# Kernel optimization log

Hardware: AMD Instinct MI355X
Metric: run time of the kernel (lower is better)

Reference implementation:

```python
import jax, jax.numpy as jnp
import numpy as np

B, N, DIM = 4, 1024, 512
H, DH = 8, 64
INNER = H * DH
MLP = 2048
EPS = 1e-5


def layernorm(x, g, b):
    m = x.mean(-1, keepdims=True)
    v = ((x - m) ** 2).mean(-1, keepdims=True)
    return (x - m) / jnp.sqrt(v + EPS) * g + b


def setup_inputs() -> dict:
    key = jax.random.key(0)
    ks = jax.random.split(key, 12)
    s = 0.02
    return {
        "q": jax.random.normal(ks[0], (B, N, DIM), jnp.float32),
        "k": jax.random.normal(ks[1], (B, N, DIM), jnp.float32),
        "v": jax.random.normal(ks[2], (B, N, DIM), jnp.float32),
        "Win": jax.random.normal(ks[3], (INNER, DIM), jnp.float32) * s,
        "Wout": jax.random.normal(ks[4], (DIM, INNER), jnp.float32) * s,
        "bout": jnp.zeros((DIM,), jnp.float32),
        "g1": jnp.ones((DIM,), jnp.float32),
        "b1n": jnp.zeros((DIM,), jnp.float32),
        "g2": jnp.ones((DIM,), jnp.float32),
        "b2n": jnp.zeros((DIM,), jnp.float32),
        "Wup": jax.random.normal(ks[5], (MLP, DIM), jnp.float32) * s,
        "bup": jnp.zeros((MLP,), jnp.float32),
        "Wdn": jax.random.normal(ks[6], (DIM, MLP), jnp.float32) * s,
        "bdn": jnp.zeros((DIM,), jnp.float32),
        "wp_W1": jax.random.normal(ks[7], (DH, 2 * DH), jnp.float32) * s,
        "wp_b1": jnp.zeros((DH,), jnp.float32),
        "wp_g": jnp.ones((DH,), jnp.float32),
        "wp_b": jnp.zeros((DH,), jnp.float32),
        "wp_W2": jax.random.normal(ks[8], (3, DH), jnp.float32) * s,
        "wp_b2": jnp.zeros((3,), jnp.float32),
        "num_heads": H,
        "dim_head": DH,
        "mlp_dim": MLP,
    }


def reference(q, k, v, Win, Wout, bout, g1, b1n, g2, b2n, Wup, bup, Wdn, bdn,
              wp_W1, wp_b1, wp_g, wp_b, wp_W2, wp_b2, num_heads, dim_head, mlp_dim):
    b, n, _ = q.shape

    def split_heads(x):  # [b,n,dim] -> [h,b,n,d]
        f = x @ Win.T
        return f.reshape(b, n, num_heads, dim_head).transpose(2, 0, 1, 3)

    fq = split_heads(layernorm(q, g1, b1n))
    fk = split_heads(layernorm(k, g1, b1n))
    fv = split_heads(layernorm(v, g1, b1n))

    # cosine similarity component
    dots = jnp.einsum('hbnd,hbmd->hbnm', fq, fk)
    nq = jnp.linalg.norm(fq, axis=-1)  # [h,b,n]
    nk = jnp.linalg.norm(fk, axis=-1)  # [h,b,m]
    cosine_sim = dots / (nq[..., :, None] * nk[..., None, :])

    # mean-centered covariance component
    qc = fq - fq.mean(-1, keepdims=True)
    kc = fk - fk.mean(-1, keepdims=True)
    cov_component = jnp.einsum('hbnd,hbmd->hbnm', qc, kc) / dim_head

    # variance outer-product component (torch.var -> unbiased, ddof=1)
    qv = jnp.var(fq, axis=-1, ddof=1)  # [h,b,n]
    kv = jnp.var(fk, axis=-1, ddof=1)  # [h,b,m]
    var_component = qv[..., :, None] * kv[..., None, :] / dim_head

    # dynamic per-head mixing weights
    qg = fq.mean(axis=(1, 2))  # [h,d]
    kg = fk.mean(axis=(1, 2))
    feats = jnp.concatenate([qg, kg], axis=-1)  # [h,2d]
    h1 = jax.nn.relu(layernorm(feats @ wp_W1.T + wp_b1, wp_g, wp_b))
    w = jax.nn.softmax(h1 @ wp_W2.T + wp_b2, axis=-1)  # [h,3]
    cw = w[:, 0][:, None, None, None]
    covw = w[:, 1][:, None, None, None]
    vw = w[:, 2][:, None, None, None]

    scores = cw * cosine_sim + covw * cov_component + vw * var_component
    out = jnp.einsum('hbnm,hbmd->hbnd', scores, fv)
    out = out.transpose(1, 2, 0, 3).reshape(b, n, num_heads * dim_head)
    attn = out @ Wout.T + bout

    q2 = q + attn
    x = layernorm(q2, g2, b2n)
    y = jax.nn.gelu(x @ Wup.T + bup, approximate=False) @ Wdn.T + bdn
    return q2 + y
```

## Files before the change

kernel.cpp:

```cpp
#include <hip/hip_runtime.h>
#include <math.h>

#define EPS 1e-5f
#define ROWS 4096

typedef __attribute__((ext_vector_type(8))) short short8;
typedef __attribute__((ext_vector_type(4))) float floatx4;

__device__ inline short f2bf(float f) {
    unsigned u = __builtin_bit_cast(unsigned, f);
    unsigned r = (u + 0x7fffu + ((u >> 16) & 1u)) >> 16;
    return (short)r;
}

__global__ __launch_bounds__(256) void prep(
    const float* __restrict__ q, const float* __restrict__ k,
    const float* __restrict__ v, const float* __restrict__ g,
    const float* __restrict__ bb, short* __restrict__ qkvout,
    const float* __restrict__ w0, const float* __restrict__ w1,
    const float* __restrict__ w2, const float* __restrict__ w3,
    short* __restrict__ o0, short* __restrict__ o1,
    short* __restrict__ o2, short* __restrict__ o3,
    float* __restrict__ zero0) {
    int bx = blockIdx.x;
    int t = threadIdx.x;
    if (bx < 3072) {
        int tensor = bx >> 10;
        int xb = bx & 1023;
        const float* x = tensor == 0 ? q : (tensor == 1 ? k : v);
        int row = xb * 4 + (t >> 6);
        int col = (t & 63) * 8;
        const float* xr = x + (size_t)row * 512 + col;
        float4 v0 = *(const float4*)xr;
        float4 v1 = *(const float4*)(xr + 4);
        float s = v0.x + v0.y + v0.z + v0.w + v1.x + v1.y + v1.z + v1.w;
        float sq = v0.x * v0.x + v0.y * v0.y + v0.z * v0.z + v0.w * v0.w +
                   v1.x * v1.x + v1.y * v1.y + v1.z * v1.z + v1.w * v1.w;
#pragma unroll
        for (int off = 32; off; off >>= 1) {
            s += __shfl_xor(s, off);
            sq += __shfl_xor(sq, off);
        }
        float m = s * (1.f / 512.f);
        float rstd = rsqrtf(sq * (1.f / 512.f) - m * m + EPS);
        float4 g0 = *(const float4*)(g + col);
        float4 g1 = *(const float4*)(g + col + 4);
        float4 b0 = *(const float4*)(bb + col);
        float4 b1 = *(const float4*)(bb + col + 4);
        short8 o;
        o[0] = f2bf((v0.x - m) * rstd * g0.x + b0.x);
        o[1] = f2bf((v0.y - m) * rstd * g0.y + b0.y);
        o[2] = f2bf((v0.z - m) * rstd * g0.z + b0.z);
        o[3] = f2bf((v0.w - m) * rstd * g0.w + b0.w);
        o[4] = f2bf((v1.x - m) * rstd * g1.x + b1.x);
        o[5] = f2bf((v1.y - m) * rstd * g1.y + b1.y);
        o[6] = f2bf((v1.z - m) * rstd * g1.z + b1.z);
        o[7] = f2bf((v1.w - m) * rstd * g1.w + b1.w);
        *(short8*)(qkvout + (size_t)(tensor * 4096 + row) * 512 + col) = o;
        return;
    }
    if (bx < 4352) {
        int wb = bx - 3072;
        const float* src;
        short* dst;
        int base;
        if (wb < 128) { src = w0; dst = o0; base = wb; }
        else if (wb < 256) { src = w1; dst = o1; base = wb - 128; }
        else if (wb < 768) { src = w2; dst = o2; base = wb - 256; }
        else { src = w3; dst = o3; base = wb - 768; }
        int idx = base * 2048 + t * 8;
        float4 v0 = *(const float4*)(src + idx);
        float4 v1 = *(const float4*)(src + idx + 4);
        short8 o;
        o[0] = f2bf(v0.x); o[1] = f2bf(v0.y); o[2] = f2bf(v0.z); o[3] = f2bf(v0.w);
        o[4] = f2bf(v1.x); o[5] = f2bf(v1.y); o[6] = f2bf(v1.z); o[7] = f2bf(v1.w);
        *(short8*)(dst + idx) = o;
        return;
    }
    int zi = (bx - 4352) * 1024 + t * 4;
    if (zi < 267264) *(float4*)(zero0 + zi) = (float4){0.f, 0.f, 0.f, 0.f};
}

template <int TM, int TN, int EPI, bool OUT_BF16>
__global__ __launch_bounds__(256) void mfma_gemm_nt(
    const short* __restrict__ A, const short* __restrict__ B,
    void* __restrict__ C, int M, int N, int K,
    const float* __restrict__ bias, const float* __restrict__ resid,
    float* __restrict__ Sb, float* __restrict__ qgp, float* __restrict__ kgp) {
    constexpr int FI = TM / 32;
    constexpr int FJ = TN / 32;
    __shared__ short As[TM * 32];
    __shared__ short Bs[TN * 32];
    int t = threadIdx.x;
    int m0 = blockIdx.y * TM, n0 = blockIdx.x * TN;
    int w = t >> 6, lane = t & 63;
    int wm = (w & 1) * (TM / 2), wn = (w >> 1) * (TN / 2);
    floatx4 acc[FI][FJ];
#pragma unroll
    for (int i = 0; i < FI; ++i)
#pragma unroll
        for (int j = 0; j < FJ; ++j) acc[i][j] = (floatx4){0.f, 0.f, 0.f, 0.f};

    int arow = t >> 2, acol = (t & 3) * 8;
    const short* Ag = A + (size_t)(m0 + arow) * K + acol;
    const short* Bg = B + (size_t)(n0 + arow) * K + acol;
    int ldsbase = w * 1024;

    for (int k0 = 0; k0 < K; k0 += 32) {
        __syncthreads();
#pragma unroll
        for (int u = 0; u < TM / 64; ++u)
            __builtin_amdgcn_global_load_lds(
                (const __attribute__((address_space(1))) void*)(Ag + (size_t)u * 64 * K + k0),
                (__attribute__((address_space(3))) void*)((char*)As + u * 4096 + ldsbase),
                16, 0, 0);
#pragma unroll
        for (int u = 0; u < TN / 64; ++u)
            __builtin_amdgcn_global_load_lds(
                (const __attribute__((address_space(1))) void*)(Bg + (size_t)u * 64 * K + k0),
                (__attribute__((address_space(3))) void*)((char*)Bs + u * 4096 + ldsbase),
                16, 0, 0);
        __syncthreads();
        int krow = (lane >> 4) * 8;
        short8 af[FI], bf[FJ];
#pragma unroll
        for (int i = 0; i < FI; ++i)
            af[i] = *(const short8*)&As[(wm + i * 16 + (lane & 15)) * 32 + krow];
#pragma unroll
        for (int j = 0; j < FJ; ++j)
            bf[j] = *(const short8*)&Bs[(wn + j * 16 + (lane & 15)) * 32 + krow];
#pragma unroll
        for (int i = 0; i < FI; ++i)
#pragma unroll
            for (int j = 0; j < FJ; ++j)
                acc[i][j] = __builtin_amdgcn_mfma_f32_16x16x32_bf16(
                    af[i], bf[j], acc[i][j], 0, 0, 0);
    }

    int col = lane & 15, rbase = (lane >> 4) * 4;
#pragma unroll
    for (int i = 0; i < FI; ++i) {
#pragma unroll
        for (int j = 0; j < FJ; ++j) {
            int gcol = n0 + wn + j * 16 + col;
#pragma unroll
            for (int r = 0; r < 4; ++r) {
                int grow = m0 + wm + i * 16 + rbase + r;
                float v = acc[i][j][r];
                if (EPI == 2) v += bias[gcol] + resid[(size_t)grow * N + gcol];
                if (EPI == 3) {
                    v += bias[gcol];
                    v = 0.5f * v * (1.f + erff(v * 0.70710678118654752f));
                }
                if (OUT_BF16)
                    ((short*)C)[(size_t)grow * N + gcol] = f2bf(v);
                else
                    ((float*)C)[(size_t)grow * N + gcol] = v;
            }
        }
    }

    if (EPI == 1) {
        if (m0 < 8192) {
            int tensor = m0 >> 12;
            float* Sbase = Sb + (size_t)tensor * 98304;
            float* dst = tensor ? kgp : qgp;
            int head = (n0 + wn) >> 6;
            int rowbase = (m0 & 4095) + wm;
#pragma unroll
            for (int i = 0; i < FI; ++i) {
#pragma unroll
                for (int r = 0; r < 4; ++r) {
                    float s = 0.f, sq = 0.f;
#pragma unroll
                    for (int j = 0; j < FJ; ++j) {
                        float vv = acc[i][j][r];
                        s += vv;
                        sq += vv * vv;
                    }
#pragma unroll
                    for (int off = 1; off < 16; off <<= 1) {
                        s += __shfl_xor(s, off);
                        sq += __shfl_xor(sq, off);
                    }
                    if ((lane & 15) == 0) {
                        int row = rowbase + i * 16 + rbase + r;
                        int idx = head * ROWS + row;
                        float m = s * (1.f / 64.f);
                        Sbase[idx] = m;
                        Sbase[32768 + idx] = rsqrtf(sq);
                        Sbase[65536 + idx] = (sq - 64.f * m * m) * (1.f / 63.f);
                    }
                }
            }
            float cs[FJ];
#pragma unroll
            for (int j = 0; j < FJ; ++j) {
                float s = 0.f;
#pragma unroll
                for (int i = 0; i < FI; ++i)
#pragma unroll
                    for (int r = 0; r < 4; ++r) s += acc[i][j][r];
                s += __shfl_xor(s, 16);
                s += __shfl_xor(s, 32);
                cs[j] = s;
            }
            if (lane < 16) {
#pragma unroll
                for (int j = 0; j < FJ; ++j)
                    atomicAdd(&dst[head * 64 + j * 16 + lane], cs[j] * (1.f / 4096.f));
            }
        }
    }
}

__global__ __launch_bounds__(256) void lnconv(
    const float* __restrict__ x, const float* __restrict__ g,
    const float* __restrict__ bb, short* __restrict__ out) {
    int t = threadIdx.x;
    int row = blockIdx.x * 4 + (t >> 6);
    int col = (t & 63) * 8;
    const float* xr = x + (size_t)row * 512 + col;
    float4 v0 = *(const float4*)xr;
    float4 v1 = *(const float4*)(xr + 4);
    float s = v0.x + v0.y + v0.z + v0.w + v1.x + v1.y + v1.z + v1.w;
    float sq = v0.x * v0.x + v0.y * v0.y + v0.z * v0.z + v0.w * v0.w +
               v1.x * v1.x + v1.y * v1.y + v1.z * v1.z + v1.w * v1.w;
#pragma unroll
    for (int off = 32; off; off >>= 1) {
        s += __shfl_xor(s, off);
        sq += __shfl_xor(sq, off);
    }
    float m = s * (1.f / 512.f);
    float rstd = rsqrtf(sq * (1.f / 512.f) - m * m + EPS);
    float4 g0 = *(const float4*)(g + col);
    float4 g1 = *(const float4*)(g + col + 4);
    float4 b0 = *(const float4*)(bb + col);
    float4 b1 = *(const float4*)(bb + col + 4);
    short8 o;
    o[0] = f2bf((v0.x - m) * rstd * g0.x + b0.x);
    o[1] = f2bf((v0.y - m) * rstd * g0.y + b0.y);
    o[2] = f2bf((v0.z - m) * rstd * g0.z + b0.z);
    o[3] = f2bf((v0.w - m) * rstd * g0.w + b0.w);
    o[4] = f2bf((v1.x - m) * rstd * g1.x + b1.x);
    o[5] = f2bf((v1.y - m) * rstd * g1.y + b1.y);
    o[6] = f2bf((v1.z - m) * rstd * g1.z + b1.z);
    o[7] = f2bf((v1.w - m) * rstd * g1.w + b1.w);
    *(short8*)(out + (size_t)row * 512 + col) = o;
}

__global__ __launch_bounds__(256) void ksideP(
    const float* __restrict__ fk, const float* __restrict__ fv,
    const float* __restrict__ rnk, const float* __restrict__ kvv,
    const float* __restrict__ mk, float* __restrict__ Mbuf,
    const float* __restrict__ qg, const float* __restrict__ kg,
    const float* __restrict__ W1, const float* __restrict__ b1,
    const float* __restrict__ g, const float* __restrict__ bb,
    const float* __restrict__ W2, const float* __restrict__ b2,
    float* __restrict__ wmix) {
    if (blockIdx.x == 32) {
        int j = threadIdx.x;
        if (j >= 64) return;
        int h = blockIdx.y;
        float acc = 0.f;
        const float* w1r = W1 + j * 128;
        for (int i = 0; i < 64; ++i) acc += qg[h * 64 + i] * w1r[i];
        for (int i = 0; i < 64; ++i) acc += kg[h * 64 + i] * w1r[64 + i];
        acc += b1[j];
        float s = acc, sq = acc * acc;
#pragma unroll
        for (int off = 32; off; off >>= 1) {
            s += __shfl_xor(s, off);
            sq += __shfl_xor(sq, off);
        }
        float m = s * (1.f / 64.f);
        float var = sq * (1.f / 64.f) - m * m;
        float xh = (acc - m) * rsqrtf(var + EPS) * g[j] + bb[j];
        float r = fmaxf(xh, 0.f);
        float l[3];
#pragma unroll
        for (int c = 0; c < 3; ++c) {
            float p = r * W2[c * 64 + j];
#pragma unroll
            for (int off = 32; off; off >>= 1) p += __shfl_xor(p, off);
            l[c] = p + b2[c];
        }
        if (j == 0) {
            float mx = fmaxf(l[0], fmaxf(l[1], l[2]));
            float e0 = expf(l[0] - mx), e1 = expf(l[1] - mx), e2 = expf(l[2] - mx);
            float inv = 1.f / (e0 + e1 + e2);
            wmix[h * 3 + 0] = e0 * inv;
            wmix[h * 3 + 1] = e1 * inv;
            wmix[h * 3 + 2] = e2 * inv;
        }
        return;
    }
    int hb = blockIdx.x;
    int chunk = blockIdx.y;
    int h = hb >> 2, b = hb & 3;
    __shared__ float fkt[2048], fvt[2048];
    __shared__ float rs[32], kvs[32], mks[32];
    int t = threadIdx.x;
    int td = t >> 4, te = t & 15;
    float m1[4][4] = {}, m2[4][4] = {};
    float skv = 0.f, smk = 0.f;
    int mstart = chunk * 128;
    for (int m0 = mstart; m0 < mstart + 128; m0 += 32) {
        __syncthreads();
#pragma unroll
        for (int u = 0; u < 2; ++u) {
            int idx = u * 1024 + t * 4;
            int mm = idx >> 6, d = idx & 63;
            size_t grow = (size_t)(b * 1024 + m0 + mm) * 512 + h * 64 + d;
            *(float4*)&fkt[idx] = *(const float4*)&fk[grow];
            *(float4*)&fvt[idx] = *(const float4*)&fv[grow];
        }
        if (t < 32) {
            int sidx = h * ROWS + b * 1024 + m0 + t;
            rs[t] = rnk[sidx];
            kvs[t] = kvv[sidx];
            mks[t] = mk[sidx];
        }
        __syncthreads();
        for (int mi = 0; mi < 32; ++mi) {
            float r = rs[mi];
            float4 kq = *(const float4*)&fkt[mi * 64 + td * 4];
            float4 vq = *(const float4*)&fvt[mi * 64 + te * 4];
            float kr[4] = {kq.x, kq.y, kq.z, kq.w};
            float vr[4] = {vq.x, vq.y, vq.z, vq.w};
#pragma unroll
            for (int i = 0; i < 4; ++i) {
                float kv_ = kr[i], krr = kv_ * r;
#pragma unroll
                for (int j = 0; j < 4; ++j) {
                    m2[i][j] += kv_ * vr[j];
                    m1[i][j] += krr * vr[j];
                }
            }
            if (t < 64) {
                skv += kvs[mi] * fvt[mi * 64 + t];
                smk += mks[mi] * fvt[mi * 64 + t];
            }
        }
    }
    float* base = Mbuf + (size_t)hb * 8320;
#pragma unroll
    for (int i = 0; i < 4; ++i)
#pragma unroll
        for (int j = 0; j < 4; ++j) {
            atomicAdd(&base[(td * 4 + i) * 64 + te * 4 + j], m1[i][j]);
            atomicAdd(&base[4096 + (td * 4 + i) * 64 + te * 4 + j], m2[i][j]);
        }
    if (t < 64) {
        atomicAdd(&base[8192 + t], skv);
        atomicAdd(&base[8256 + t], smk);
    }
}

__global__ __launch_bounds__(256) void qside(
    const float* __restrict__ fq, const float* __restrict__ Mbuf,
    const float* __restrict__ rnq, const float* __restrict__ mq,
    const float* __restrict__ qv, const float* __restrict__ wmix,
    short* __restrict__ attn_out) {
    int ntile = blockIdx.x, hb = blockIdx.y;
    int h = hb >> 2, b = hb & 3;
    __shared__ float M1s[4096], M2s[4096], fqt[4096];
    __shared__ float Skvs[64], Smks[64], rnqs[64], mqs[64], qvs[64];
    int t = threadIdx.x;
    const float* base = Mbuf + (size_t)hb * 8320;
#pragma unroll
    for (int u = 0; u < 4; ++u) {
        int idx = t * 4 + u * 1024;
        *(float4*)&M1s[idx] = *(const float4*)&base[idx];
        *(float4*)&M2s[idx] = *(const float4*)&base[4096 + idx];
    }
    int n0 = ntile * 64;
#pragma unroll
    for (int u = 0; u < 4; ++u) {
        int idx = t * 4 + u * 1024;
        int r = idx >> 6, d = idx & 63;
        *(float4*)&fqt[idx] = *(const float4*)&fq[(size_t)(b * 1024 + n0 + r) * 512 + h * 64 + d];
    }
    if (t < 64) {
        Skvs[t] = base[8192 + t];
        Smks[t] = base[8256 + t];
        int sidx = h * ROWS + b * 1024 + n0 + t;
        rnqs[t] = rnq[sidx];
        mqs[t] = mq[sidx];
        qvs[t] = qv[sidx];
    }
    __syncthreads();
    float cw = wmix[h * 3 + 0], covw = wmix[h * 3 + 1], vw = wmix[h * 3 + 2];
    int e = t & 63, rq = t >> 6;
    float a1[16] = {}, a2[16] = {};
    for (int d4 = 0; d4 < 64; d4 += 4) {
        float md1[4], md2[4];
#pragma unroll
        for (int dd = 0; dd < 4; ++dd) {
            md1[dd] = M1s[(d4 + dd) * 64 + e];
            md2[dd] = M2s[(d4 + dd) * 64 + e];
        }
#pragma unroll
        for (int i = 0; i < 16; ++i) {
            float4 f = *(const float4*)&fqt[(rq * 16 + i) * 64 + d4];
            a1[i] += f.x * md1[0] + f.y * md1[1] + f.z * md1[2] + f.w * md1[3];
            a2[i] += f.x * md2[0] + f.y * md2[1] + f.z * md2[2] + f.w * md2[3];
        }
    }
    float c2 = covw * (1.f / 64.f), c3 = vw * (1.f / 64.f);
#pragma unroll
    for (int i = 0; i < 16; ++i) {
        int rr = rq * 16 + i;
        float v = cw * rnqs[rr] * a1[i] + c2 * a2[i] + c3 * qvs[rr] * Skvs[e] -
                  covw * mqs[rr] * Smks[e];
        attn_out[(size_t)(b * 1024 + n0 + rr) * 512 + h * 64 + e] = f2bf(v);
    }
}

extern "C" void kernel_launch(void* const* d_in, const int* in_sizes, int n_in,
                              void* d_out, int out_size, void* d_ws, size_t ws_size,
                              hipStream_t stream) {
    const float* q = (const float*)d_in[0];
    const float* k = (const float*)d_in[1];
    const float* v = (const float*)d_in[2];
    const float* Win = (const float*)d_in[3];
    const float* Wout = (const float*)d_in[4];
    const float* bout = (const float*)d_in[5];
    const float* g1 = (const float*)d_in[6];
    const float* b1n = (const float*)d_in[7];
    const float* g2 = (const float*)d_in[8];
    const float* b2n = (const float*)d_in[9];
    const float* Wup = (const float*)d_in[10];
    const float* bup = (const float*)d_in[11];
    const float* Wdn = (const float*)d_in[12];
    const float* bdn = (const float*)d_in[13];
    const float* wpW1 = (const float*)d_in[14];
    const float* wpb1 = (const float*)d_in[15];
    const float* wpg = (const float*)d_in[16];
    const float* wpb = (const float*)d_in[17];
    const float* wpW2 = (const float*)d_in[18];
    const float* wpb2 = (const float*)d_in[19];
    float* out = (float*)d_out;

    float* wsf = (float*)d_ws;
    float* fq = wsf;
    float* fk = wsf + 2097152;
    float* fv = wsf + 2 * 2097152;
    short* hmid = (short*)wsf;
    short* qkvln = (short*)(wsf + 6291456);
    short* attnbf = (short*)(wsf + 6291456);
    short* x2bf = (short*)(wsf + 6291456 + 1048576);
    short* Winbf = (short*)(wsf + 9437184);
    short* Woutbf = (short*)(wsf + 9437184 + 131072);
    short* Wupbf = (short*)(wsf + 9437184 + 262144);
    short* Wdnbf = (short*)(wsf + 9437184 + 262144 + 524288);
    float* S = wsf + 10747904;
    float* qg = S + 196608;
    float* kg = qg + 512;
    float* Mbuf = kg + 512;
    float* wmix = Mbuf + 266240;
    float* mqS = S, *rnqS = S + 32768, *qvS = S + 65536;
    float* mkS = S + 98304, *rnkS = S + 131072, *kvS = S + 163840;

    prep<<<4613, 256, 0, stream>>>(q, k, v, g1, b1n, qkvln,
                                   Win, Wout, Wup, Wdn,
                                   Winbf, Woutbf, Wupbf, Wdnbf, qg);

    mfma_gemm_nt<64, 128, 1, false><<<dim3(4, 192), 256, 0, stream>>>(
        qkvln, Winbf, fq, 12288, 512, 512, nullptr, nullptr, S, qg, kg);

    ksideP<<<dim3(33, 8), 256, 0, stream>>>(fk, fv, rnkS, kvS, mkS, Mbuf,
                                            qg, kg, wpW1, wpb1, wpg, wpb,
                                            wpW2, wpb2, wmix);

    qside<<<dim3(16, 32), 256, 0, stream>>>(fq, Mbuf, rnqS, mqS, qvS, wmix, attnbf);

    mfma_gemm_nt<64, 64, 2, false><<<dim3(8, 64), 256, 0, stream>>>(
        attnbf, Woutbf, out, 4096, 512, 512, bout, q, nullptr, nullptr, nullptr);

    lnconv<<<1024, 256, 0, stream>>>(out, g2, b2n, x2bf);
    mfma_gemm_nt<64, 128, 3, true><<<dim3(16, 64), 256, 0, stream>>>(
        x2bf, Wupbf, hmid, 4096, 2048, 512, bup, nullptr, nullptr, nullptr, nullptr);
    mfma_gemm_nt<64, 128, 2, false><<<dim3(4, 64), 256, 0, stream>>>(
        hmid, Wdnbf, out, 4096, 512, 2048, bdn, out, nullptr, nullptr, nullptr);
}
```

Before: 274.2 us.

## Split K-side outer-product reduction into bf16 transpose pass plus MFMA GEMM

Replaces the scalar FP32 K^T V accumulation kernel with two kernels. The first transposes fk (raw and norm-scaled) and fv into bf16 buffers and computes the per-column vector sums. The second runs the 64x64 K^T V products as split-K MFMA GEMMs with atomic accumulation. The aim is to move the outer-product work onto matrix cores, at the cost of an extra launch, an extra round trip through global memory, and bf16 rounding of those intermediates. The zero-initialisation of the new Mnew/Sv buffers is not visible here, so whether they start cleared is unverified.

```diff
diff --git a/kernel.cpp b/kernel.cpp
--- a/kernel.cpp
+++ b/kernel.cpp
@@ -249,19 +249,21 @@
     *(short8*)(out + (size_t)row * 512 + col) = o;
 }
 
-__global__ __launch_bounds__(256) void ksideP(
+__global__ __launch_bounds__(256) void tr_kv(
     const float* __restrict__ fk, const float* __restrict__ fv,
     const float* __restrict__ rnk, const float* __restrict__ kvv,
-    const float* __restrict__ mk, float* __restrict__ Mbuf,
+    const float* __restrict__ mkm, short* __restrict__ fkTall,
+    short* __restrict__ fvT, float* __restrict__ Sv,
     const float* __restrict__ qg, const float* __restrict__ kg,
     const float* __restrict__ W1, const float* __restrict__ b1,
     const float* __restrict__ g, const float* __restrict__ bb,
     const float* __restrict__ W2, const float* __restrict__ b2,
     float* __restrict__ wmix) {
-    if (blockIdx.x == 32) {
-        int j = threadIdx.x;
-        if (j >= 64) return;
-        int h = blockIdx.y;
+    int hb = blockIdx.x;
+    int t = threadIdx.x;
+    if (blockIdx.y == 8) {
+        if (blockIdx.z != 0 || hb >= 8 || t >= 64) return;
+        int h = hb, j = t;
         float acc = 0.f;
         const float* w1r = W1 + j * 128;
         for (int i = 0; i < 64; ++i) acc += qg[h * 64 + i] * w1r[i];
@@ -295,84 +297,136 @@
         }
         return;
     }
-    int hb = blockIdx.x;
     int chunk = blockIdx.y;
+    int tensor = blockIdx.z;
     int h = hb >> 2, b = hb & 3;
-    __shared__ float fkt[2048], fvt[2048];
-    __shared__ float rs[32], kvs[32], mks[32];
-    int t = threadIdx.x;
-    int td = t >> 4, te = t & 15;
-    float m1[4][4] = {}, m2[4][4] = {};
-    float skv = 0.f, smk = 0.f;
-    int mstart = chunk * 128;
-    for (int m0 = mstart; m0 < mstart + 128; m0 += 32) {
+    __shared__ float tile[32][68];
+    __shared__ float sc[32], sc2[32];
+    const float* src = tensor ? fv : fk;
+    float skv_acc = 0.f, smk_acc = 0.f;
+    int e = t & 63, qd = t >> 6;
+    int d = t >> 2, mg = (t & 3) * 8;
+    for (int s4 = 0; s4 < 4; ++s4) {
+        int m0 = chunk * 128 + s4 * 32;
         __syncthreads();
 #pragma unroll
         for (int u = 0; u < 2; ++u) {
             int idx = u * 1024 + t * 4;
-            int mm = idx >> 6, d = idx & 63;
-            size_t grow = (size_t)(b * 1024 + m0 + mm) * 512 + h * 64 + d;
-            *(float4*)&fkt[idx] = *(const float4*)&fk[grow];
-            *(float4*)&fvt[idx] = *(const float4*)&fv[grow];
+            int mm = idx >> 6, dd = idx & 63;
+            *(float4*)&tile[mm][dd] =
+                *(const float4*)&src[(size_t)(b * 1024 + m0 + mm) * 512 + h * 64 + dd];
         }
         if (t < 32) {
             int sidx = h * ROWS + b * 1024 + m0 + t;
-            rs[t] = rnk[sidx];
-            kvs[t] = kvv[sidx];
-            mks[t] = mk[sidx];
+            if (tensor == 0) {
+                sc[t] = rnk[sidx];
+            } else {
+                sc[t] = kvv[sidx];
+                sc2[t] = mkm[sidx];
+            }
         }
         __syncthreads();
-        for (int mi = 0; mi < 32; ++mi) {
-            float r = rs[mi];
-            float4 kq = *(const float4*)&fkt[mi * 64 + td * 4];
-            float4 vq = *(const float4*)&fvt[mi * 64 + te * 4];
-            float kr[4] = {kq.x, kq.y, kq.z, kq.w};
-            float vr[4] = {vq.x, vq.y, vq.z, vq.w};
-#pragma unroll
-            for (int i = 0; i < 4; ++i) {
-                float kv_ = kr[i], krr = kv_ * r;
-#pragma unroll
-                for (int j = 0; j < 4; ++j) {
-                    m2[i][j] += kv_ * vr[j];
-                    m1[i][j] += krr * vr[j];
-                }
-            }
-            if (t < 64) {
-                skv += kvs[mi] * fvt[mi * 64 + t];
-                smk += mks[mi] * fvt[mi * 64 + t];
-            }
-        }
-    }
-    float* base = Mbuf + (size_t)hb * 8320;
-#pragma unroll
-    for (int i = 0; i < 4; ++i)
-#pragma unroll
-        for (int j = 0; j < 4; ++j) {
-            atomicAdd(&base[(td * 4 + i) * 64 + te * 4 + j], m1[i][j]);
-            atomicAdd(&base[4096 + (td * 4 + i) * 64 + te * 4 + j], m2[i][j]);
-        }
-    if (t < 64) {
-        atomicAdd(&base[8192 + t], skv);
-        atomicAdd(&base[8256 + t], smk);
-    }
+        if (tensor == 0) {
+            short8 o1, o2;
+#pragma unroll
+            for (int i = 0; i < 8; ++i) {
+                float vv = tile[mg + i][d];
+                o1[i] = f2bf(vv);
+                o2[i] = f2bf(vv * sc[mg + i]);
+            }
+            *(short8*)&fkTall[((size_t)hb * 128 + d) * 1024 + m0 + mg] = o1;
+            *(short8*)&fkTall[((size_t)hb * 128 + 64 + d) * 1024 + m0 + mg] = o2;
+        } else {
+            short8 o1;
+#pragma unroll
+            for (int i = 0; i < 8; ++i) o1[i] = f2bf(tile[mg + i][d]);
+            *(short8*)&fvT[((size_t)hb * 64 + d) * 1024 + m0 + mg] = o1;
+#pragma unroll
+            for (int i = 0; i < 8; ++i) {
+                float vv = tile[qd * 8 + i][e];
+                skv_acc += sc[qd * 8 + i] * vv;
+                smk_acc += sc2[qd * 8 + i] * vv;
+            }
+        }
+    }
+    if (tensor == 1) {
+        atomicAdd(&Sv[hb * 128 + e], skv_acc);
+        atomicAdd(&Sv[hb * 128 + 64 + e], smk_acc);
+    }
+}
+
+__global__ __launch_bounds__(256) void kside_gemm(
+    const short* __restrict__ fkTall, const short* __restrict__ fvT,
+    float* __restrict__ Mnew) {
+    int hb = blockIdx.x, half = blockIdx.y, kz = blockIdx.z;
+    const short* A = fkTall + ((size_t)hb * 128 + half * 64) * 1024 + kz * 256;
+    const short* B = fvT + (size_t)hb * 64 * 1024 + kz * 256;
+    __shared__ short As[64 * 32];
+    __shared__ short Bs[64 * 32];
+    int t = threadIdx.x;
+    int w = t >> 6, lane = t & 63;
+    int wm = (w & 1) * 32, wn = (w >> 1) * 32;
+    floatx4 acc[2][2];
+#pragma unroll
+    for (int i = 0; i < 2; ++i)
+#pragma unroll
+        for (int j = 0; j < 2; ++j) acc[i][j] = (floatx4){0.f, 0.f, 0.f, 0.f};
+    int arow = t >> 2, acol = (t & 3) * 8;
+    const short* Ag = A + (size_t)arow * 1024 + acol;
+    const short* Bg = B + (size_t)arow * 1024 + acol;
+    int ldsbase = w * 1024;
+    for (int k0 = 0; k0 < 256; k0 += 32) {
+        __syncthreads();
+        __builtin_amdgcn_global_load_lds(
+            (const __attribute__((address_space(1))) void*)(Ag + k0),
+            (__attribute__((address_space(3))) void*)((char*)As + ldsbase), 16, 0, 0);
+        __builtin_amdgcn_global_load_lds(
+            (const __attribute__((address_space(1))) void*)(Bg + k0),
+            (__attribute__((address_space(3))) void*)((char*)Bs + ldsbase), 16, 0, 0);
+        __syncthreads();
+        int krow = (lane >> 4) * 8;
+        short8 af[2], bf[2];
+#pragma unroll
+        for (int i = 0; i < 2; ++i)
+            af[i] = *(const short8*)&As[(wm + i * 16 + (lane & 15)) * 32 + krow];
+#pragma unroll
+        for (int j = 0; j < 2; ++j)
+            bf[j] = *(const short8*)&Bs[(wn + j * 16 + (lane & 15)) * 32 + krow];
+#pragma unroll
+        for (int i = 0; i < 2; ++i)
+#pragma unroll
+            for (int j = 0; j < 2; ++j)
+                acc[i][j] = __builtin_amdgcn_mfma_f32_16x16x32_bf16(
+                    af[i], bf[j], acc[i][j], 0, 0, 0);
+    }
+    int col = lane & 15, rbase = (lane >> 4) * 4;
+    float* Cb = Mnew + (size_t)hb * 8192 + half * 4096;
+#pragma unroll
+    for (int i = 0; i < 2; ++i)
+#pragma unroll
+        for (int j = 0; j < 2; ++j)
+#pragma unroll
+            for (int r = 0; r < 4; ++r)
+                atomicAdd(&Cb[(wm + i * 16 + rbase + r) * 64 + wn + j * 16 + col],
+                          acc[i][j][r]);
 }
 
 __global__ __launch_bounds__(256) void qside(
-    const float* __restrict__ fq, const float* __restrict__ Mbuf,
-    const float* __restrict__ rnq, const float* __restrict__ mq,
-    const float* __restrict__ qv, const float* __restrict__ wmix,
-    short* __restrict__ attn_out) {
+    const float* __restrict__ fq, const float* __restrict__ Mnew,
+    const float* __restrict__ Sv, const float* __restrict__ rnq,
+    const float* __restrict__ mq, const float* __restrict__ qv,
+    const float* __restrict__ wmix, short* __restrict__ attn_out) {
     int ntile = blockIdx.x, hb = blockIdx.y;
     int h = hb >> 2, b = hb & 3;
     __shared__ float M1s[4096], M2s[4096], fqt[4096];
     __shared__ float Skvs[64], Smks[64], rnqs[64], mqs[64], qvs[64];
     int t = threadIdx.x;
-    const float* base = Mbuf + (size_t)hb * 8320;
+    const float* base = Mnew + (size_t)hb * 8192;
 #pragma unroll
     for (int u = 0; u < 4; ++u) {
         int idx = t * 4 + u * 1024;
-        *(float4*)&M1s[idx] = *(const float4*)&base[idx];
-        *(float4*)&M2s[idx] = *(const float4*)&base[4096 + idx];
+        *(float4*)&M2s[idx] = *(const float4*)&base[idx];
+        *(float4*)&M1s[idx] = *(const float4*)&base[4096 + idx];
     }
     int n0 = ntile * 64;
 #pragma unroll
@@ -382,8 +436,8 @@
         *(float4*)&fqt[idx] = *(const float4*)&fq[(size_t)(b * 1024 + n0 + r) * 512 + h * 64 + d];
     }
     if (t < 64) {
-        Skvs[t] = base[8192 + t];
-        Smks[t] = base[8256 + t];
+        Skvs[t] = Sv[hb * 128 + t];
+        Smks[t] = Sv[hb * 128 + 64 + t];
         int sidx = h * ROWS + b * 1024 + n0 + t;
         rnqs[t] = rnq[sidx];
         mqs[t] = mq[sidx];
@@ -448,6 +502,8 @@
     float* fv = wsf + 2 * 2097152;
     short* hmid = (short*)wsf;
     short* qkvln = (short*)(wsf + 6291456);
+    short* fkTall = (short*)(wsf + 6291456);
+    short* fvT = (short*)(wsf + 8388608);
     short* attnbf = (short*)(wsf + 6291456);
     short* x2bf = (short*)(wsf + 6291456 + 1048576);
     short* Winbf = (short*)(wsf + 9437184);
@@ -457,8 +513,9 @@
     float* S = wsf + 10747904;
     float* qg = S + 196608;
     float* kg = qg + 512;
-    float* Mbuf = kg + 512;
-    float* wmix = Mbuf + 266240;
+    float* Mnew = kg + 512;
+    float* Sv = Mnew + 262144;
+    float* wmix = Sv + 4096;
     float* mqS = S, *rnqS = S + 32768, *qvS = S + 65536;
     float* mkS = S + 98304, *rnkS = S + 131072, *kvS = S + 163840;
 
@@ -469,11 +526,15 @@
     mfma_gemm_nt<64, 128, 1, false><<<dim3(4, 192), 256, 0, stream>>>(
         qkvln, Winbf, fq, 12288, 512, 512, nullptr, nullptr, S, qg, kg);
 
-    ksideP<<<dim3(33, 8), 256, 0, stream>>>(fk, fv, rnkS, kvS, mkS, Mbuf,
-                                            qg, kg, wpW1, wpb1, wpg, wpb,
-                                            wpW2, wpb2, wmix);
-
-    qside<<<dim3(16, 32), 256, 0, stream>>>(fq, Mbuf, rnqS, mqS, qvS, wmix, attnbf);
+    tr_kv<<<dim3(32, 9, 2), 256, 0, stream>>>(fk, fv, rnkS, kvS, mkS,
+                                              fkTall, fvT, Sv,
+                                              qg, kg, wpW1, wpb1, wpg, wpb,
+                                              wpW2, wpb2, wmix);
+
+    kside_gemm<<<dim3(32, 2, 4), 256, 0, stream>>>(fkTall, fvT, Mnew);
+
+    qside<<<dim3(16, 32), 256, 0, stream>>>(fq, Mnew, Sv, rnqS, mqS, qvS,
+                                            wmix, attnbf);
 
     mfma_gemm_nt<64, 64, 2, false><<<dim3(8, 64), 256, 0, stream>>>(
         attnbf, Woutbf, out, 4096, 512, 512, bout, q, nullptr, nullptr, nullptr);
```

Measured after the change: 242.5 us. -11.6%, faster.
